# Kernel tuning notes

Measured on AMD Instinct MI355X. Metric: run time of the kernel, lower is better.

The kernel has to match this reference:

```python
import jax, jax.numpy as jnp
import numpy as np

N = 100000
E = 1600000
IN_CH = 64
HID = 32


def _gatv2(x, src, dst, wl, bl, wr, br, att, bias, heads, out_ch, concat):
    # GATv2Conv (PyG semantics, share_weights=False, negative_slope=0.2,
    # self-loops already appended to src/dst by caller).
    n = x.shape[0]
    xl = (x @ wl + bl).reshape(n, heads, out_ch)  # source transform
    xr = (x @ wr + br).reshape(n, heads, out_ch)  # target transform
    xj = xl[src]                                   # [E, H, C]
    xi = xr[dst]
    e = jax.nn.leaky_relu(xi + xj, negative_slope=0.2)
    alpha = jnp.einsum('ehc,hc->eh', e, att)       # [E, H]
    amax = jax.ops.segment_max(alpha, dst, num_segments=n)
    alpha = jnp.exp(alpha - amax[dst])
    denom = jax.ops.segment_sum(alpha, dst, num_segments=n)
    alpha = alpha / (denom[dst] + 1e-16)
    out = jax.ops.segment_sum(alpha[:, :, None] * xj, dst, num_segments=n)
    out = out.reshape(n, heads * out_ch) if concat else out.mean(axis=1)
    return out + bias


def setup_inputs() -> dict:
    key = jax.random.key(0)
    ks = jax.random.split(key, 20)
    s = 0.1
    d = {
        'x': jax.random.normal(ks[0], (N, IN_CH), jnp.float32),
        'edge_index': jax.random.randint(ks[1], (2, E), 0, N, jnp.int32),
        # conv1: in=64 -> heads=4, C=32, concat
        'w1l': s * jax.random.normal(ks[2], (IN_CH, 4 * HID), jnp.float32),
        'b1l': jnp.zeros((4 * HID,), jnp.float32),
        'w1r': s * jax.random.normal(ks[3], (IN_CH, 4 * HID), jnp.float32),
        'b1r': jnp.zeros((4 * HID,), jnp.float32),
        'a1': s * jax.random.normal(ks[4], (4, HID), jnp.float32),
        'c1': jnp.zeros((4 * HID,), jnp.float32),
        # conv2: in=128 -> heads=2, C=32, concat
        'w2l': s * jax.random.normal(ks[5], (4 * HID, 2 * HID), jnp.float32),
        'b2l': jnp.zeros((2 * HID,), jnp.float32),
        'w2r': s * jax.random.normal(ks[6], (4 * HID, 2 * HID), jnp.float32),
        'b2r': jnp.zeros((2 * HID,), jnp.float32),
        'a2': s * jax.random.normal(ks[7], (2, HID), jnp.float32),
        'c2': jnp.zeros((2 * HID,), jnp.float32),
        # conv3: in=64 -> heads=1, C=32, mean (concat=False)
        'w3l': s * jax.random.normal(ks[8], (2 * HID, HID), jnp.float32),
        'b3l': jnp.zeros((HID,), jnp.float32),
        'w3r': s * jax.random.normal(ks[9], (2 * HID, HID), jnp.float32),
        'b3r': jnp.zeros((HID,), jnp.float32),
        'a3': s * jax.random.normal(ks[10], (1, HID), jnp.float32),
        'c3': jnp.zeros((HID,), jnp.float32),
        # MLP head 32 -> 16 -> 2
        'wm1': s * jax.random.normal(ks[11], (HID, HID // 2), jnp.float32),
        'bm1': jnp.zeros((HID // 2,), jnp.float32),
        'wm2': s * jax.random.normal(ks[12], (HID // 2, 2), jnp.float32),
        'bm2': jnp.zeros((2,), jnp.float32),
    }
    return d


def reference(x, edge_index,
              w1l, b1l, w1r, b1r, a1, c1,
              w2l, b2l, w2r, b2r, a2, c2,
              w3l, b3l, w3r, b3r, a3, c3,
              wm1, bm1, wm2, bm2):
    n = x.shape[0]
    loop = jnp.arange(n, dtype=edge_index.dtype)
    src = jnp.concatenate([edge_index[0], loop])  # add_self_loops=True (PyG default)
    dst = jnp.concatenate([edge_index[1], loop])
    h = jax.nn.relu(_gatv2(x, src, dst, w1l, b1l, w1r, b1r, a1, c1, 4, HID, True))
    h = jax.nn.relu(_gatv2(h, src, dst, w2l, b2l, w2r, b2r, a2, c2, 2, HID, True))
    h = jax.nn.relu(_gatv2(h, src, dst, w3l, b3l, w3r, b3r, a3, c3, 1, HID, False))
    raw = jax.nn.relu(h @ wm1 + bm1) @ wm2 + bm2
    v_mag = jax.nn.sigmoid(raw[:, 0]) + 0.5
    v_angle = jnp.tanh(raw[:, 1]) * 180.0
    return jnp.stack([v_mag, v_angle], axis=1)
```

## Files before the change

### kernel.cpp

```cpp
#include <hip/hip_runtime.h>
#include <hip/hip_fp16.h>


constexpr int N = 100000;
constexpr int E = 1600000;
constexpr int S = 48;

constexpr int NBUK = (N + 127) >> 7;
constexpr int BCAP = 384;
constexpr int BIN_B = (E + 1023) / 1024;
constexpr int XMM_B = (N + 63) / 64;

typedef _Float16 half8_t __attribute__((ext_vector_type(8)));
typedef _Float16 half4_t __attribute__((ext_vector_type(4)));
typedef _Float16 h2 __attribute__((ext_vector_type(2)));
typedef float f32x4 __attribute__((ext_vector_type(4)));


__global__ __launch_bounds__(256) void k_bin(const int* __restrict__ ei,
                                             int* __restrict__ bcnt,
                                             unsigned* __restrict__ bbuf) {
  const int base = blockIdx.x * 1024 + threadIdx.x;
  const int cls = blockIdx.x & 7;
  unsigned ent[4];
  int idx[4];
  bool ok[4];
  #pragma unroll
  for (int j = 0; j < 4; ++j) {
    int e = base + j * 256;
    ok[j] = e < E;
    int ec = ok[j] ? e : 0;
    int src = ei[ec];
    int dst = ei[E + ec];
    idx[j] = (dst >> 7) * 8 + cls;
    ent[j] = ((unsigned)(dst & 127) << 17) | (unsigned)src;
  }
  int pos[4];
  #pragma unroll
  for (int j = 0; j < 4; ++j) {
    pos[j] = ok[j] ? atomicAdd(&bcnt[idx[j]], 1) : BCAP;
  }
  #pragma unroll
  for (int j = 0; j < 4; ++j) {
    if (pos[j] < BCAP) bbuf[(size_t)idx[j] * BCAP + pos[j]] = ent[j];
  }
}


__global__ __launch_bounds__(256) void k_insert(const int* __restrict__ bcnt,
                                                const unsigned* __restrict__ bbuf,
                                                int* __restrict__ deg,
                                                int* __restrict__ ebuf) {
  __shared__ int cnt[128];
  const int b = blockIdx.x;
  const int tid = threadIdx.x;
  const int node0 = b * 128 + tid;
  if (tid < 128) {
    cnt[tid] = 1;
    if (node0 < N) ebuf[node0 * S] = node0;
  }
  __syncthreads();
  #pragma unroll 1
  for (int c = 0; c < 8; ++c) {
    const int n = min(bcnt[b * 8 + c], BCAP);
    const unsigned* arr = bbuf + (size_t)(b * 8 + c) * BCAP;
    for (int i = tid; i < n; i += 256) {
      const unsigned ent = arr[i];
      const int dlo = (int)(ent >> 17);
      const int src = (int)(ent & 0x1FFFFu);
      const int pos = atomicAdd(&cnt[dlo], 1);
      if (pos < S) ebuf[(b * 128 + dlo) * S + pos] = src;
    }
  }
  __syncthreads();
  if (tid < 128 && node0 < N) deg[node0] = cnt[tid];
}


template <int K, int M>
__device__ __forceinline__ void wprep_body(const float* __restrict__ src,
                                           __half* __restrict__ dst, int blk) {
  const int idx = blk * 256 + threadIdx.x;
  const int k = idx / M;
  const int m = idx % M;
  ((_Float16*)dst)[m * K + (k ^ ((m & 7) << 3))] = (_Float16)src[idx];
}

__global__ __launch_bounds__(256) void k_wprep(
    const float* w1l, const float* w1r, const float* w2l, const float* w2r,
    const float* w3l, const float* w3r,
    __half* o1l, __half* o1r, __half* o2l, __half* o2r,
    __half* o3l, __half* o3r) {
  int b = blockIdx.x;
  if      (b < 32)  wprep_body<64, 128>(w1l, o1l, b);
  else if (b < 64)  wprep_body<64, 128>(w1r, o1r, b - 32);
  else if (b < 96)  wprep_body<128, 64>(w2l, o2l, b - 64);
  else if (b < 128) wprep_body<128, 64>(w2r, o2r, b - 96);
  else if (b < 136) wprep_body<64, 32>(w3l, o3l, b - 128);
  else              wprep_body<64, 32>(w3r, o3r, b - 136);
}


template <int K, int M>
__global__ __launch_bounds__(256) void k_xmm(const float* __restrict__ x,
                                             const __half* __restrict__ wtl,
                                             const __half* __restrict__ wtr,
                                             const float* __restrict__ bl,
                                             const float* __restrict__ br,
                                             __half* __restrict__ Aout,
                                             __half* __restrict__ Bout) {
  constexpr int XSZ = 64 * K;
  constexpr int WSZ = M * K;
  constexpr int KS = K / 32;
  constexpr int CT = M / 16;
  __shared__ _Float16 pool[XSZ + 2 * WSZ];

  const int tid = threadIdx.x;
  const int node0 = blockIdx.x * 64;

  for (int i = tid; i < 64 * (K / 4); i += 256) {
    const int row = i / (K / 4);
    const int c4 = i % (K / 4);
    const int grow = min(node0 + row, N - 1);
    float4 v = reinterpret_cast<const float4*>(x)[(size_t)grow * (K / 4) + c4];
    const int k0 = c4 * 4;
    const int hidx = row * K + ((k0) ^ ((row & 7) << 3));
    *reinterpret_cast<half4_t*>(&pool[hidx]) =
        (half4_t){(_Float16)v.x, (_Float16)v.y, (_Float16)v.z, (_Float16)v.w};
  }
  for (int i = tid; i < WSZ / 8; i += 256) {
    reinterpret_cast<uint4*>(&pool[XSZ])[i] =
        reinterpret_cast<const uint4*>(wtl)[i];
    reinterpret_cast<uint4*>(&pool[XSZ + WSZ])[i] =
        reinterpret_cast<const uint4*>(wtr)[i];
  }
  __syncthreads();

  const int lane = tid & 63;
  const int wid = tid >> 6;
  const int r0 = wid * 16;

  half8_t af[KS];
  #pragma unroll
  for (int ks = 0; ks < KS; ++ks) {
    const int row = r0 + (lane & 15);
    const int k0 = ks * 32 + (lane >> 4) * 8;
    af[ks] = *reinterpret_cast<const half8_t*>(
        &pool[row * K + (k0 ^ ((row & 7) << 3))]);
  }

  f32x4 accl[CT], accr[CT];
  #pragma unroll
  for (int ct = 0; ct < CT; ++ct) {
    accl[ct] = (f32x4){0.f, 0.f, 0.f, 0.f};
    accr[ct] = (f32x4){0.f, 0.f, 0.f, 0.f};
  }

  #pragma unroll
  for (int ct = 0; ct < CT; ++ct) {
    #pragma unroll
    for (int ks = 0; ks < KS; ++ks) {
      const int col = ct * 16 + (lane & 15);
      const int k0 = ks * 32 + (lane >> 4) * 8;
      const int hb = col * K + (k0 ^ ((col & 7) << 3));
      half8_t bfl = *reinterpret_cast<const half8_t*>(&pool[XSZ + hb]);
      accl[ct] = __builtin_amdgcn_mfma_f32_16x16x32_f16(af[ks], bfl, accl[ct], 0, 0, 0);
      half8_t bfr = *reinterpret_cast<const half8_t*>(&pool[XSZ + WSZ + hb]);
      accr[ct] = __builtin_amdgcn_mfma_f32_16x16x32_f16(af[ks], bfr, accr[ct], 0, 0, 0);
    }
  }

  __syncthreads();
  #pragma unroll
  for (int ct = 0; ct < CT; ++ct) {
    const int col = ct * 16 + (lane & 15);
    const float bb = bl[col];
    #pragma unroll
    for (int r = 0; r < 4; ++r) {
      const int row = r0 + (lane >> 4) * 4 + r;
      pool[row * M + col] = (_Float16)(accl[ct][r] + bb);
    }
  }
  __syncthreads();
  for (int i = tid; i < 64 * (M / 8); i += 256) {
    const int row = i / (M / 8);
    const int j = i % (M / 8);
    const int g = node0 + row;
    if (g < N)
      reinterpret_cast<uint4*>(Aout + (size_t)g * M)[j] =
          reinterpret_cast<uint4*>(&pool[row * M])[j];
  }
  __syncthreads();
  #pragma unroll
  for (int ct = 0; ct < CT; ++ct) {
    const int col = ct * 16 + (lane & 15);
    const float bb = br[col];
    #pragma unroll
    for (int r = 0; r < 4; ++r) {
      const int row = r0 + (lane >> 4) * 4 + r;
      pool[row * M + col] = (_Float16)(accr[ct][r] + bb);
    }
  }
  __syncthreads();
  for (int i = tid; i < 64 * (M / 8); i += 256) {
    const int row = i / (M / 8);
    const int j = i % (M / 8);
    const int g = node0 + row;
    if (g < N)
      reinterpret_cast<uint4*>(Bout + (size_t)g * M)[j] =
          reinterpret_cast<uint4*>(&pool[row * M])[j];
  }
}


template <int CTRL>
__device__ __forceinline__ float dpp_add(float x) {
  return x + __builtin_bit_cast(float,
      __builtin_amdgcn_update_dpp(0, __builtin_bit_cast(int, x),
                                  CTRL, 0xF, 0xF, true));
}

template <int H>
__global__ __launch_bounds__(256) void k_gat(const __half* __restrict__ xl,
                                             const __half* __restrict__ xr,
                                             const float* __restrict__ att,
                                             const float* __restrict__ bias,
                                             const int* __restrict__ deg,
                                             const int* __restrict__ ebuf,
                                             float* __restrict__ out) {
  constexpr int F = H * 32;
  constexpr int F8 = F / 8;
  constexpr int F4 = F / 4;
  constexpr int LPE = F8;
  constexpr int EPI = 64 / LPE;
  constexpr float LOG2E = 1.44269504088896f;
  const int lane = threadIdx.x & 63;
  const int node = (blockIdx.x * blockDim.x + threadIdx.x) >> 6;
  if (node >= N) return;
  const int li = lane & (LPE - 1);
  const int eg = lane / LPE;

  const uint4* xl4 = reinterpret_cast<const uint4*>(xl);
  const uint4* xr4 = reinterpret_cast<const uint4*>(xr);

  const uint4 xiraw = xr4[(unsigned)node * F8 + li];
  h2 xi2[4];
  xi2[0] = __builtin_bit_cast(h2, xiraw.x);
  xi2[1] = __builtin_bit_cast(h2, xiraw.y);
  xi2[2] = __builtin_bit_cast(h2, xiraw.z);
  xi2[3] = __builtin_bit_cast(h2, xiraw.w);

  const float4 at0 = reinterpret_cast<const float4*>(att)[li * 2];
  const float4 at1 = reinterpret_cast<const float4*>(att)[li * 2 + 1];
  h2 at2[4];
  at2[0] = (h2){(_Float16)(at0.x * LOG2E), (_Float16)(at0.y * LOG2E)};
  at2[1] = (h2){(_Float16)(at0.z * LOG2E), (_Float16)(at0.w * LOG2E)};
  at2[2] = (h2){(_Float16)(at1.x * LOG2E), (_Float16)(at1.y * LOG2E)};
  at2[3] = (h2){(_Float16)(at1.z * LOG2E), (_Float16)(at1.w * LOG2E)};
  const h2 c02 = {(_Float16)0.2f, (_Float16)0.2f};

  float4 acc0 = make_float4(0.f, 0.f, 0.f, 0.f);
  float4 acc1 = make_float4(0.f, 0.f, 0.f, 0.f);
  float l = 0.f;

  const int* row = ebuf + node * S;
  const int dn = min(deg[node], S);
  const int last = dn - 1;
  const int iters = (dn + EPI - 1) / EPI;

  auto process = [&](const uint4& raw, bool valid) {
    h2 xj0 = __builtin_bit_cast(h2, raw.x);
    h2 xj1 = __builtin_bit_cast(h2, raw.y);
    h2 xj2 = __builtin_bit_cast(h2, raw.z);
    h2 xj3 = __builtin_bit_cast(h2, raw.w);
    float t = 0.f;
    h2 v;
    v = xi2[0] + xj0; v = __builtin_elementwise_max(v, v * c02);
    t = __builtin_amdgcn_fdot2(at2[0], v, t, false);
    v = xi2[1] + xj1; v = __builtin_elementwise_max(v, v * c02);
    t = __builtin_amdgcn_fdot2(at2[1], v, t, false);
    v = xi2[2] + xj2; v = __builtin_elementwise_max(v, v * c02);
    t = __builtin_amdgcn_fdot2(at2[2], v, t, false);
    v = xi2[3] + xj3; v = __builtin_elementwise_max(v, v * c02);
    t = __builtin_amdgcn_fdot2(at2[3], v, t, false);
    t = dpp_add<0xB1>(t);
    t = dpp_add<0x4E>(t);
    float pm = valid ? exp2f(t) : 0.f;
    l += pm;
    acc0.x = fmaf(pm, (float)xj0[0], acc0.x);
    acc0.y = fmaf(pm, (float)xj0[1], acc0.y);
    acc0.z = fmaf(pm, (float)xj1[0], acc0.z);
    acc0.w = fmaf(pm, (float)xj1[1], acc0.w);
    acc1.x = fmaf(pm, (float)xj2[0], acc1.x);
    acc1.y = fmaf(pm, (float)xj2[1], acc1.y);
    acc1.z = fmaf(pm, (float)xj3[0], acc1.z);
    acc1.w = fmaf(pm, (float)xj3[1], acc1.w);
  };

  int i = eg;
  bool vA = i < dn;
  int s0 = row[min(i, last)];
  i += EPI;
  uint4 xjA = xl4[(unsigned)s0 * F8 + li];
  bool vB = i < dn;
  int sN = row[min(i, last)];
  i += EPI;
  uint4 xjB;

  for (int it = 0; it < iters; it += 2) {
    xjB = xl4[(unsigned)sN * F8 + li];
    bool vn = i < dn;
    sN = row[min(i, last)];
    i += EPI;
    process(xjA, vA);
    vA = vn;
    xjA = xl4[(unsigned)sN * F8 + li];
    vn = i < dn;
    sN = row[min(i, last)];
    i += EPI;
    process(xjB, vB);
    vB = vn;
  }

  #pragma unroll
  for (int ofs = LPE; ofs < 64; ofs <<= 1) {
    acc0.x += __shfl_xor(acc0.x, ofs);
    acc0.y += __shfl_xor(acc0.y, ofs);
    acc0.z += __shfl_xor(acc0.z, ofs);
    acc0.w += __shfl_xor(acc0.w, ofs);
    acc1.x += __shfl_xor(acc1.x, ofs);
    acc1.y += __shfl_xor(acc1.y, ofs);
    acc1.z += __shfl_xor(acc1.z, ofs);
    acc1.w += __shfl_xor(acc1.w, ofs);
    l      += __shfl_xor(l, ofs);
  }

  if (lane < LPE) {
    const float inv = 1.f / (l + 1e-16f);
    const float4 bv0 = reinterpret_cast<const float4*>(bias)[li * 2];
    const float4 bv1 = reinterpret_cast<const float4*>(bias)[li * 2 + 1];
    float4 r0, r1;
    r0.x = fmaxf(acc0.x * inv + bv0.x, 0.f);
    r0.y = fmaxf(acc0.y * inv + bv0.y, 0.f);
    r0.z = fmaxf(acc0.z * inv + bv0.z, 0.f);
    r0.w = fmaxf(acc0.w * inv + bv0.w, 0.f);
    r1.x = fmaxf(acc1.x * inv + bv1.x, 0.f);
    r1.y = fmaxf(acc1.y * inv + bv1.y, 0.f);
    r1.z = fmaxf(acc1.z * inv + bv1.z, 0.f);
    r1.w = fmaxf(acc1.w * inv + bv1.w, 0.f);
    float4* op = reinterpret_cast<float4*>(out) + (unsigned)node * F4 + li * 2;
    op[0] = r0;
    op[1] = r1;
  }
}


__global__ __launch_bounds__(256) void k_mlp(const float* __restrict__ h,
                                             const float* __restrict__ wm1,
                                             const float* __restrict__ bm1,
                                             const float* __restrict__ wm2,
                                             const float* __restrict__ bm2,
                                             float* __restrict__ out) {
  __shared__ float w1[512], b1[16], w2[32], b2[2];
  const int tid = threadIdx.x;
  for (int i = tid; i < 512; i += 256) w1[i] = wm1[i];
  if (tid < 16) b1[tid] = bm1[tid];
  if (tid < 32) w2[tid] = wm2[tid];
  if (tid < 2)  b2[tid] = bm2[tid];
  __syncthreads();
  const int node = blockIdx.x * blockDim.x + tid;
  if (node >= N) return;
  float hv[32];
  const float* hp = h + (size_t)node * 32;
  #pragma unroll
  for (int k = 0; k < 8; ++k) {
    float4 v = reinterpret_cast<const float4*>(hp)[k];
    hv[4 * k] = v.x; hv[4 * k + 1] = v.y; hv[4 * k + 2] = v.z; hv[4 * k + 3] = v.w;
  }
  float r0 = b2[0], r1 = b2[1];
  #pragma unroll
  for (int j = 0; j < 16; ++j) {
    float a = b1[j];
    #pragma unroll
    for (int k = 0; k < 32; ++k) a += hv[k] * w1[k * 16 + j];
    a = fmaxf(a, 0.f);
    r0 += a * w2[j * 2];
    r1 += a * w2[j * 2 + 1];
  }
  float vm = 1.f / (1.f + __expf(-r0)) + 0.5f;
  float va = tanhf(r1) * 180.f;
  out[(size_t)node * 2]     = vm;
  out[(size_t)node * 2 + 1] = va;
}


extern "C" void kernel_launch(void* const* d_in, const int* in_sizes, int n_in,
                              void* d_out, int out_size, void* d_ws, size_t ws_size,
                              hipStream_t stream) {
  const float* x   = (const float*)d_in[0];
  const int*   ei  = (const int*)d_in[1];
  const float* w1l = (const float*)d_in[2];
  const float* b1l = (const float*)d_in[3];
  const float* w1r = (const float*)d_in[4];
  const float* b1r = (const float*)d_in[5];
  const float* a1  = (const float*)d_in[6];
  const float* c1  = (const float*)d_in[7];
  const float* w2l = (const float*)d_in[8];
  const float* b2l = (const float*)d_in[9];
  const float* w2r = (const float*)d_in[10];
  const float* b2r = (const float*)d_in[11];
  const float* a2  = (const float*)d_in[12];
  const float* c2  = (const float*)d_in[13];
  const float* w3l = (const float*)d_in[14];
  const float* b3l = (const float*)d_in[15];
  const float* w3r = (const float*)d_in[16];
  const float* b3r = (const float*)d_in[17];
  const float* a3  = (const float*)d_in[18];
  const float* c3  = (const float*)d_in[19];
  const float* wm1 = (const float*)d_in[20];
  const float* bm1 = (const float*)d_in[21];
  const float* wm2 = (const float*)d_in[22];
  const float* bm2 = (const float*)d_in[23];
  float* outp = (float*)d_out;
  (void)in_sizes; (void)n_in; (void)out_size; (void)ws_size;

  char* ws = (char*)d_ws;
  size_t o = 0;
  auto take = [&](size_t bytes) {
    char* p = ws + o;
    o = (o + bytes + 255) & ~(size_t)255;
    return p;
  };
  int* deg       = (int*)take((size_t)N * sizeof(int));
  int* ebuf      = (int*)take((size_t)N * S * sizeof(int));
  int* bcnt      = (int*)take((size_t)NBUK * 8 * sizeof(int));
  unsigned* bbuf = (unsigned*)take((size_t)NBUK * 8 * BCAP * sizeof(unsigned));
  __half* A      = (__half*)take((size_t)N * 128 * sizeof(__half));
  __half* B      = (__half*)take((size_t)N * 128 * sizeof(__half));
  float* Cb      = (float*)take((size_t)N * 128 * sizeof(float));
  __half* t1l    = (__half*)take(128 * 64 * sizeof(__half));
  __half* t1r    = (__half*)take(128 * 64 * sizeof(__half));
  __half* t2l    = (__half*)take(64 * 128 * sizeof(__half));
  __half* t2r    = (__half*)take(64 * 128 * sizeof(__half));
  __half* t3l    = (__half*)take(32 * 64 * sizeof(__half));
  __half* t3r    = (__half*)take(32 * 64 * sizeof(__half));

  hipMemsetAsync(bcnt, 0, (size_t)NBUK * 8 * sizeof(int), stream);
  k_wprep<<<144, 256, 0, stream>>>(w1l, w1r, w2l, w2r, w3l, w3r,
                                   t1l, t1r, t2l, t2r, t3l, t3r);
  k_bin<<<BIN_B, 256, 0, stream>>>(ei, bcnt, bbuf);
  k_insert<<<NBUK, 256, 0, stream>>>(bcnt, bbuf, deg, ebuf);

  k_xmm<64, 128><<<XMM_B, 256, 0, stream>>>(x, t1l, t1r, b1l, b1r, A, B);
  k_gat<4><<<N / 4, 256, 0, stream>>>(A, B, a1, c1, deg, ebuf, Cb);

  k_xmm<128, 64><<<XMM_B, 256, 0, stream>>>(Cb, t2l, t2r, b2l, b2r, A, B);
  k_gat<2><<<N / 4, 256, 0, stream>>>(A, B, a2, c2, deg, ebuf, Cb);

  k_xmm<64, 32><<<XMM_B, 256, 0, stream>>>(Cb, t3l, t3r, b3l, b3r, A, B);
  k_gat<1><<<N / 4, 256, 0, stream>>>(A, B, a3, c3, deg, ebuf, Cb);

  k_mlp<<<(N + 255) / 256, 256, 0, stream>>>(Cb, wm1, bm1, wm2, bm2, outp);
}
```

Before: 436.7 us.

## Aggregate bucket counts in shared-memory histogram before global atomics in binning

The binning kernel now has each block handle 8192 edges. It first counts edges per destination bucket in a shared-memory histogram, then reserves space with one global atomic per non-empty bucket, then scatters entries using shared-memory atomics for the slot positions. The aim is to replace one global atomic per edge with far fewer global atomics. The cost is that the destination indices are read twice, and there are fewer blocks (about 196) with a large shared array.

```diff
diff --git a/kernel.cpp b/kernel.cpp
--- a/kernel.cpp
+++ b/kernel.cpp
@@ -8,7 +8,8 @@
 
 constexpr int NBUK = (N + 127) >> 7;
 constexpr int BCAP = 384;
-constexpr int BIN_B = (E + 1023) / 1024;
+constexpr int EPB = 8192;
+constexpr int BIN_B = (E + EPB - 1) / EPB;
 constexpr int XMM_B = (N + 63) / 64;
 
 typedef _Float16 half8_t __attribute__((ext_vector_type(8)));
@@ -20,29 +21,35 @@
 __global__ __launch_bounds__(256) void k_bin(const int* __restrict__ ei,
                                              int* __restrict__ bcnt,
                                              unsigned* __restrict__ bbuf) {
-  const int base = blockIdx.x * 1024 + threadIdx.x;
+  __shared__ int hist[NBUK];
+  const int tid = threadIdx.x;
   const int cls = blockIdx.x & 7;
-  unsigned ent[4];
-  int idx[4];
-  bool ok[4];
-  #pragma unroll
-  for (int j = 0; j < 4; ++j) {
-    int e = base + j * 256;
-    ok[j] = e < E;
-    int ec = ok[j] ? e : 0;
-    int src = ei[ec];
-    int dst = ei[E + ec];
-    idx[j] = (dst >> 7) * 8 + cls;
-    ent[j] = ((unsigned)(dst & 127) << 17) | (unsigned)src;
-  }
-  int pos[4];
-  #pragma unroll
-  for (int j = 0; j < 4; ++j) {
-    pos[j] = ok[j] ? atomicAdd(&bcnt[idx[j]], 1) : BCAP;
-  }
-  #pragma unroll
-  for (int j = 0; j < 4; ++j) {
-    if (pos[j] < BCAP) bbuf[(size_t)idx[j] * BCAP + pos[j]] = ent[j];
+  const int e0 = blockIdx.x * EPB;
+  for (int i = tid; i < NBUK; i += 256) hist[i] = 0;
+  __syncthreads();
+  #pragma unroll 4
+  for (int j = 0; j < EPB / 256; ++j) {
+    const int e = e0 + j * 256 + tid;
+    if (e < E) atomicAdd(&hist[ei[E + e] >> 7], 1);
+  }
+  __syncthreads();
+  for (int i = tid; i < NBUK; i += 256) {
+    const int h = hist[i];
+    hist[i] = h ? atomicAdd(&bcnt[i * 8 + cls], h) : 0;
+  }
+  __syncthreads();
+  #pragma unroll 4
+  for (int j = 0; j < EPB / 256; ++j) {
+    const int e = e0 + j * 256 + tid;
+    if (e < E) {
+      const int src = ei[e];
+      const int dst = ei[E + e];
+      const int b = dst >> 7;
+      const int pos = atomicAdd(&hist[b], 1);
+      if (pos < BCAP)
+        bbuf[(size_t)(b * 8 + cls) * BCAP + pos] =
+            ((unsigned)(dst & 127) << 17) | (unsigned)src;
+    }
   }
 }
 
```

Result: faster. 392.6 us (-10.1%).
